# Kernel optimization log

Measured on AMD Instinct MI355X. Metric: run time of the kernel, lower is better.

Reference implementation:

```python
import jax, jax.numpy as jnp
import numpy as np

D = 128
EPS = 1e-5

def group_norm1(x, gamma, beta):
    # GroupNorm with num_groups=1 over channel dim of [N, C]
    mu = jnp.mean(x, axis=-1, keepdims=True)
    var = jnp.mean(jnp.square(x - mu), axis=-1, keepdims=True)
    xhat = (x - mu) * jax.lax.rsqrt(var + EPS)
    return xhat * gamma + beta

def setup_inputs() -> dict:
    key = jax.random.key(0)
    ks = jax.random.split(key, 12)
    N_ctx, N_tgt, E = 40000, 40000, 640000
    s = 0.09  # ~1/sqrt(128) weight scale
    inp = {
        'context_feat': jax.random.normal(ks[0], (N_ctx, D), jnp.float32),
        'target_feat': jax.random.normal(ks[1], (N_tgt, D), jnp.float32),
        'context_pose': jax.random.normal(ks[2], (N_ctx, 4), jnp.float32),
        'target_pose': jax.random.normal(ks[3], (N_tgt, 4), jnp.float32),
        'W_input': s * jax.random.normal(ks[4], (D, D), jnp.float32),
        'W_rp': 0.5 * jax.random.normal(ks[5], (4, D), jnp.float32),
        'b_rp': jnp.zeros((D,), jnp.float32),
        'W_c1': s * jax.random.normal(ks[6], (2 * D, D), jnp.float32),
        'g_c1': jnp.ones((D,), jnp.float32),
        'b_c1': jnp.zeros((D,), jnp.float32),
        'W_c2': s * jax.random.normal(ks[7], (D, D), jnp.float32),
        'g_n': jnp.ones((D,), jnp.float32),
        'b_n': jnp.zeros((D,), jnp.float32),
        'W_m1': s * jax.random.normal(ks[8], (D, D), jnp.float32),
        'g_m1': jnp.ones((D,), jnp.float32),
        'bm1': jnp.zeros((D,), jnp.float32),
        'W_m2': s * jax.random.normal(ks[9], (D, D), jnp.float32),
        'g_m2': jnp.ones((D,), jnp.float32),
        'bm2': jnp.zeros((D,), jnp.float32),
        'hi': jax.random.randint(ks[10], (E,), 0, N_ctx, jnp.int32),
        'wi': jax.random.randint(ks[11], (E,), 0, N_tgt, jnp.int32),
    }
    return inp

def reference(context_feat, target_feat, context_pose, target_pose,
              W_input, W_rp, b_rp, W_c1, g_c1, b_c1, W_c2,
              g_n, b_n, W_m1, g_m1, bm1, W_m2, g_m2, bm2, hi, wi):
    # relpose: Linear(4,128) + ReLU on relative pose of each (context, target) edge
    dist_feat = context_pose[hi] - target_pose[wi]                 # [E, 4]
    dist_feat = jax.nn.relu(dist_feat @ W_rp + b_rp)               # [E, 128]
    # ctx: Linear(256,128,GN,ReLU) -> Linear(128,128, no bias)
    ctx = jnp.concatenate([context_feat[hi], dist_feat], axis=-1)  # [E, 256]
    ctx = jax.nn.relu(group_norm1(ctx @ W_c1, g_c1, b_c1))
    ctx = ctx @ W_c2                                               # [E, 128]
    # input linear + index_add scatter into targets
    tf = target_feat @ W_input                                     # [N_tgt, 128]
    tf = tf + jax.ops.segment_sum(ctx, wi, num_segments=target_feat.shape[0])
    tf = jax.nn.relu(group_norm1(tf, g_n, b_n))
    # mlp: Linear(GN,ReLU) -> Linear(GN, no act)
    tf = jax.nn.relu(group_norm1(tf @ W_m1, g_m1, bm1))
    tf = group_norm1(tf @ W_m2, g_m2, bm2)
    # residual + relu
    return jax.nn.relu(tf + target_feat)
```

## Files before the change

### kernel.cpp

```cpp
#include <hip/hip_runtime.h>

#define D 128
#define EPSV 1e-5f

typedef __attribute__((ext_vector_type(8))) __bf16 bf16x8;
typedef __attribute__((ext_vector_type(4))) float f32x4;

__device__ __forceinline__ ushort f2bf(float x) {
  unsigned u = __float_as_uint(x);
  u += 0x7fffu + ((u >> 16) & 1u);
  return (ushort)(u >> 16);
}
__device__ __forceinline__ unsigned cvtpk(float lo, float hi) {
  unsigned r;
  asm("v_cvt_pk_bf16_f32 %0, %1, %2" : "=v"(r) : "v"(lo), "v"(hi));
  return r;
}
__device__ __forceinline__ int yidx(int row, int col) {
  return row * 128 + (col ^ ((row & 7) << 3));
}

__global__ void k_cvt(const float* __restrict__ Wc1, const float* __restrict__ Wc2,
                      ushort* __restrict__ WF1, ushort* __restrict__ WF2) {
  int o = blockIdx.x * 256 + threadIdx.x;
  if (o < 32768) {
    int j = o & 7, col = (o >> 3) & 127, gg = (o >> 10) & 3, kc = o >> 12;
    WF1[o] = f2bf(Wc1[(kc * 32 + gg * 8 + j) * 128 + col]);
  } else {
    int o2 = o - 32768;
    if (o2 < 16384) {
      int j = o2 & 7, col = (o2 >> 3) & 127, gg = (o2 >> 10) & 3, kc = o2 >> 12;
      WF2[o2] = f2bf(Wc2[(kc * 32 + gg * 8 + j) * 128 + col]);
    }
  }
}

__global__ void k_cvtf(const float* __restrict__ cf, ushort* __restrict__ cb,
                       int n8) {
  int i = blockIdx.x * 256 + threadIdx.x;
  if (i < n8) {
    float4 f0 = *(const float4*)(cf + (size_t)i * 8);
    float4 f1 = *(const float4*)(cf + (size_t)i * 8 + 4);
    uint4 p;
    p.x = cvtpk(f0.x, f0.y); p.y = cvtpk(f0.z, f0.w);
    p.z = cvtpk(f1.x, f1.y); p.w = cvtpk(f1.z, f1.w);
    *(uint4*)(cb + (size_t)i * 8) = p;
  }
}

__global__ void k_hist(const int* __restrict__ hi, int* __restrict__ hist, int E) {
  int i = blockIdx.x * 256 + threadIdx.x;
  if (i < E) atomicAdd(&hist[hi[i]], 1);
}

__global__ void k_scan1(const int* __restrict__ hist, int* __restrict__ bsum, int Nc) {
  __shared__ int sd[256];
  int t = threadIdx.x, i = blockIdx.x * 256 + t;
  sd[t] = (i < Nc) ? hist[i] : 0;
  __syncthreads();
  for (int off = 128; off > 0; off >>= 1) {
    if (t < off) sd[t] += sd[t + off];
    __syncthreads();
  }
  if (t == 0) bsum[blockIdx.x] = sd[0];
}

__global__ void k_scan2(const int* __restrict__ bsum, int* __restrict__ bpre, int nc) {
  __shared__ int sd[256];
  int t = threadIdx.x;
  int v = (t < nc) ? bsum[t] : 0;
  sd[t] = v;
  __syncthreads();
  for (int off = 1; off < 256; off <<= 1) {
    int x = (t >= off) ? sd[t - off] : 0;
    __syncthreads();
    sd[t] += x;
    __syncthreads();
  }
  if (t < nc) bpre[t] = sd[t] - v;
}

__global__ void k_scan3(const int* __restrict__ hist, const int* __restrict__ bpre,
                        int* __restrict__ cursor, int Nc) {
  __shared__ int sd[256];
  int t = threadIdx.x, i = blockIdx.x * 256 + t;
  int v = (i < Nc) ? hist[i] : 0;
  sd[t] = v;
  __syncthreads();
  for (int off = 1; off < 256; off <<= 1) {
    int x = (t >= off) ? sd[t - off] : 0;
    __syncthreads();
    sd[t] += x;
    __syncthreads();
  }
  if (i < Nc) cursor[i] = bpre[blockIdx.x] + sd[t] - v;
}

__global__ void k_order(const int* __restrict__ hi, const int* __restrict__ wi,
                        int* __restrict__ cursor,
                        int* __restrict__ hs, int* __restrict__ wt, int E) {
  int i = blockIdx.x * 256 + threadIdx.x;
  if (i < E) {
    int h = hi[i];
    int p = atomicAdd(&cursor[h], 1);
    hs[p] = h;
    wt[p] = wi[i];
  }
}

template <bool BF16CF>
__global__ __launch_bounds__(256, 4) void k_edge(
    const float* __restrict__ cfeat, const ushort* __restrict__ cfb,
    const float* __restrict__ cpose, const float* __restrict__ tpose,
    const float* __restrict__ Wrp, const float* __restrict__ brp,
    const float* __restrict__ gc1, const float* __restrict__ bc1,
    const ushort* __restrict__ WF1, const ushort* __restrict__ WF2,
    const int* __restrict__ he, const int* __restrict__ we,
    float* __restrict__ acc, int E) {
  __shared__ ushort Ybuf[128 * 128];
  __shared__ float gnbuf[2][128][2];
  __shared__ int wl[128];

  const int t = threadIdx.x;
  const int lane = t & 63;
  const int wv = t >> 6;
  const int wm = wv >> 1, wn = wv & 1;
  const int s = lane & 15, g = lane >> 4;
  const int e0 = blockIdx.x * 128;

  if (t < 128) wl[t] = we[min(e0 + t, E - 1)];

  int hl[4];
#pragma unroll
  for (int m = 0; m < 4; ++m)
    hl[m] = he[min(e0 + wm * 64 + m * 16 + s, E - 1)];

  {
    const int e = t >> 1;
    const int jh = (t & 1) * 64;
    const int ge = min(e0 + e, E - 1);
    const int h = he[ge], w = we[ge];
    float4 cp = *(const float4*)(cpose + (size_t)h * 4);
    float4 tp = *(const float4*)(tpose + (size_t)w * 4);
    const float d0 = cp.x - tp.x, d1 = cp.y - tp.y;
    const float d2 = cp.z - tp.z, d3 = cp.w - tp.w;
#pragma unroll
    for (int q = 0; q < 16; ++q) {
      const int j = jh + q * 4;
      float4 b  = *(const float4*)(brp + j);
      float4 w0 = *(const float4*)(Wrp + j);
      float4 w1 = *(const float4*)(Wrp + D + j);
      float4 w2 = *(const float4*)(Wrp + 2 * D + j);
      float4 w3 = *(const float4*)(Wrp + 3 * D + j);
      float r0 = fmaxf(b.x + d0 * w0.x + d1 * w1.x + d2 * w2.x + d3 * w3.x, 0.f);
      float r1 = fmaxf(b.y + d0 * w0.y + d1 * w1.y + d2 * w2.y + d3 * w3.y, 0.f);
      float r2 = fmaxf(b.z + d0 * w0.z + d1 * w1.z + d2 * w2.z + d3 * w3.z, 0.f);
      float r3 = fmaxf(b.w + d0 * w0.w + d1 * w1.w + d2 * w2.w + d3 * w3.w, 0.f);
      *(uint2*)&Ybuf[yidx(e, j)] = make_uint2(cvtpk(r0, r1), cvtpk(r2, r3));
    }
  }

  auto bfrag = [&](const ushort* WF, int kc, int n) {
    return *(const bf16x8*)&WF[(((kc * 4 + g) * 128) + wn * 64 + n * 16 + s) * 8];
  };

  f32x4 acc1[4][4];
#pragma unroll
  for (int m = 0; m < 4; ++m)
#pragma unroll
    for (int n = 0; n < 4; ++n) acc1[m][n] = (f32x4){0.f, 0.f, 0.f, 0.f};

  for (int kc = 0; kc < 4; ++kc) {
    bf16x8 a[4];
    if (BF16CF) {
#pragma unroll
      for (int m = 0; m < 4; ++m)
        a[m] = *(const bf16x8*)(cfb + (size_t)hl[m] * D + kc * 32 + g * 8);
    } else {
#pragma unroll
      for (int m = 0; m < 4; ++m) {
        const float* src = cfeat + (size_t)hl[m] * D + kc * 32 + g * 8;
        float4 f0 = *(const float4*)src;
        float4 f1 = *(const float4*)(src + 4);
        union { uint4 u; bf16x8 v; } cv;
        cv.u.x = cvtpk(f0.x, f0.y); cv.u.y = cvtpk(f0.z, f0.w);
        cv.u.z = cvtpk(f1.x, f1.y); cv.u.w = cvtpk(f1.z, f1.w);
        a[m] = cv.v;
      }
    }
#pragma unroll
    for (int n = 0; n < 4; ++n) {
      bf16x8 b = bfrag(WF1, kc, n);
#pragma unroll
      for (int m = 0; m < 4; ++m)
        acc1[m][n] =
            __builtin_amdgcn_mfma_f32_16x16x32_bf16(a[m], b, acc1[m][n], 0, 0, 0);
    }
  }

  __syncthreads();

  for (int kc = 4; kc < 8; ++kc) {
    bf16x8 a[4];
#pragma unroll
    for (int m = 0; m < 4; ++m)
      a[m] = *(const bf16x8*)
          &Ybuf[yidx(wm * 64 + m * 16 + s, (kc - 4) * 32 + g * 8)];
#pragma unroll
    for (int n = 0; n < 4; ++n) {
      bf16x8 b = bfrag(WF1, kc, n);
#pragma unroll
      for (int m = 0; m < 4; ++m)
        acc1[m][n] =
            __builtin_amdgcn_mfma_f32_16x16x32_bf16(a[m], b, acc1[m][n], 0, 0, 0);
    }
  }

#pragma unroll
  for (int m = 0; m < 4; ++m) {
#pragma unroll
    for (int reg = 0; reg < 4; ++reg) {
      float p1 = acc1[m][0][reg] + acc1[m][1][reg] + acc1[m][2][reg] +
                 acc1[m][3][reg];
      float p2 = acc1[m][0][reg] * acc1[m][0][reg] +
                 acc1[m][1][reg] * acc1[m][1][reg] +
                 acc1[m][2][reg] * acc1[m][2][reg] +
                 acc1[m][3][reg] * acc1[m][3][reg];
#pragma unroll
      for (int msk = 1; msk < 16; msk <<= 1) {
        p1 += __shfl_xor(p1, msk, 64);
        p2 += __shfl_xor(p2, msk, 64);
      }
      if (s == 0) {
        const int row = wm * 64 + m * 16 + g * 4 + reg;
        *(float2*)&gnbuf[wn][row][0] = make_float2(p1, p2);
      }
    }
  }
  __syncthreads();

  {
    float gcl[4], bcl[4];
#pragma unroll
    for (int n = 0; n < 4; ++n) {
      gcl[n] = gc1[wn * 64 + n * 16 + s];
      bcl[n] = bc1[wn * 64 + n * 16 + s];
    }
#pragma unroll
    for (int m = 0; m < 4; ++m) {
#pragma unroll
      for (int reg = 0; reg < 4; ++reg) {
        const int row = wm * 64 + m * 16 + g * 4 + reg;
        float2 q0 = *(const float2*)&gnbuf[0][row][0];
        float2 q1 = *(const float2*)&gnbuf[1][row][0];
        const float mean = (q0.x + q1.x) * (1.f / 128.f);
        const float var = (q0.y + q1.y) * (1.f / 128.f) - mean * mean;
        const float rstd = rsqrtf(var + EPSV);
#pragma unroll
        for (int n = 0; n < 4; ++n) {
          float y = fmaxf((acc1[m][n][reg] - mean) * rstd * gcl[n] + bcl[n], 0.f);
          Ybuf[yidx(row, wn * 64 + n * 16 + s)] = (ushort)cvtpk(y, y);
        }
      }
    }
  }
  __syncthreads();

  f32x4 acc2[4][4];
#pragma unroll
  for (int m = 0; m < 4; ++m)
#pragma unroll
    for (int n = 0; n < 4; ++n) acc2[m][n] = (f32x4){0.f, 0.f, 0.f, 0.f};

  for (int kc = 0; kc < 4; ++kc) {
    bf16x8 a[4];
#pragma unroll
    for (int m = 0; m < 4; ++m)
      a[m] = *(const bf16x8*)&Ybuf[yidx(wm * 64 + m * 16 + s, kc * 32 + g * 8)];
#pragma unroll
    for (int n = 0; n < 4; ++n) {
      bf16x8 b = bfrag(WF2, kc, n);
#pragma unroll
      for (int m = 0; m < 4; ++m)
        acc2[m][n] =
            __builtin_amdgcn_mfma_f32_16x16x32_bf16(a[m], b, acc2[m][n], 0, 0, 0);
    }
  }

#pragma unroll
  for (int m = 0; m < 4; ++m) {
#pragma unroll
    for (int reg = 0; reg < 4; ++reg) {
      const int rl = wm * 64 + m * 16 + g * 4 + reg;
      if (e0 + rl < E) {
        const int w = wl[rl];
        float* base = acc + (size_t)w * D + wn * 64 + s;
#pragma unroll
        for (int n = 0; n < 4; ++n)
          unsafeAtomicAdd(base + n * 16, acc2[m][n][reg]);
      }
    }
  }
}

__device__ __forceinline__ void reduce16(float& a, float& b) {
#pragma unroll
  for (int w = 1; w < 16; w <<= 1) {
    a += __shfl_xor(a, w, 64);
    b += __shfl_xor(b, w, 64);
  }
}

__global__ __launch_bounds__(256, 2) void k_input(
    const float* __restrict__ tfeat, const float* __restrict__ Wi,
    float* __restrict__ acc, int N) {
  __shared__ float Wbuf[64][132];
  __shared__ float xt[64][132];
  const int t = threadIdx.x;
  const int r = t >> 4, s = t & 15, j0 = s * 8;
  const int row0 = blockIdx.x * 64;

  for (int idx = t; idx < 64 * 32; idx += 256) {
    int rr = idx >> 5, c4 = idx & 31;
    int grow = row0 + rr;
    float4 v = make_float4(0.f, 0.f, 0.f, 0.f);
    if (grow < N) v = *(const float4*)(tfeat + (size_t)grow * D + c4 * 4);
    *(float4*)&xt[rr][c4 * 4] = v;
  }

  float a[4][8] = {};
  for (int kc = 0; kc < 2; ++kc) {
    __syncthreads();
    for (int idx = t; idx < 64 * 32; idx += 256) {
      int kk = idx >> 5, c4 = idx & 31;
      *(float4*)&Wbuf[kk][c4 * 4] =
          *(const float4*)(Wi + (size_t)(kc * 64 + kk) * D + c4 * 4);
    }
    __syncthreads();
#pragma unroll 4
    for (int kk = 0; kk < 64; ++kk) {
      float4 w0 = *(const float4*)&Wbuf[kk][j0];
      float4 w1 = *(const float4*)&Wbuf[kk][j0 + 4];
#pragma unroll
      for (int i = 0; i < 4; ++i) {
        float xv = xt[r + 16 * i][kc * 64 + kk];
        a[i][0] += xv * w0.x; a[i][1] += xv * w0.y;
        a[i][2] += xv * w0.z; a[i][3] += xv * w0.w;
        a[i][4] += xv * w1.x; a[i][5] += xv * w1.y;
        a[i][6] += xv * w1.z; a[i][7] += xv * w1.w;
      }
    }
  }
#pragma unroll
  for (int i = 0; i < 4; ++i) {
    int row = row0 + r + 16 * i;
    if (row < N) {
      *(float4*)(acc + (size_t)row * D + j0) =
          make_float4(a[i][0], a[i][1], a[i][2], a[i][3]);
      *(float4*)(acc + (size_t)row * D + j0 + 4) =
          make_float4(a[i][4], a[i][5], a[i][6], a[i][7]);
    }
  }
}

__global__ __launch_bounds__(256, 2) void k_node(
    const float* __restrict__ tfeat,
    const float* __restrict__ gn, const float* __restrict__ bn,
    const float* __restrict__ Wm1, const float* __restrict__ gm1,
    const float* __restrict__ bm1,
    const float* __restrict__ Wm2, const float* __restrict__ gm2,
    const float* __restrict__ bm2,
    float* __restrict__ acc, int N) {
  __shared__ float Wbuf[64][132];
  __shared__ float xt[64][132];
  const int t = threadIdx.x;
  const int r = t >> 4, s = t & 15, j0 = s * 8;
  const int row0 = blockIdx.x * 64;

  auto stageW = [&](const float* W, int kc) {
    for (int idx = t; idx < 64 * 32; idx += 256) {
      int kk = idx >> 5, c4 = idx & 31;
      *(float4*)&Wbuf[kk][c4 * 4] =
          *(const float4*)(W + (size_t)(kc * 64 + kk) * D + c4 * 4);
    }
  };
  auto gemm = [&](float (&a)[4][8], int kc) {
#pragma unroll 4
    for (int kk = 0; kk < 64; ++kk) {
      float4 w0 = *(const float4*)&Wbuf[kk][j0];
      float4 w1 = *(const float4*)&Wbuf[kk][j0 + 4];
#pragma unroll
      for (int i = 0; i < 4; ++i) {
        float xv = xt[r + 16 * i][kc * 64 + kk];
        a[i][0] += xv * w0.x; a[i][1] += xv * w0.y;
        a[i][2] += xv * w0.z; a[i][3] += xv * w0.w;
        a[i][4] += xv * w1.x; a[i][5] += xv * w1.y;
        a[i][6] += xv * w1.z; a[i][7] += xv * w1.w;
      }
    }
  };

  {
    float gv[8], bv[8];
#pragma unroll
    for (int m = 0; m < 8; ++m) { gv[m] = gn[j0 + m]; bv[m] = bn[j0 + m]; }
#pragma unroll
    for (int i = 0; i < 4; ++i) {
      int row = row0 + r + 16 * i;
      float v[8] = {};
      if (row < N) {
        float4 v0 = *(const float4*)(acc + (size_t)row * D + j0);
        float4 v1 = *(const float4*)(acc + (size_t)row * D + j0 + 4);
        v[0] = v0.x; v[1] = v0.y; v[2] = v0.z; v[3] = v0.w;
        v[4] = v1.x; v[5] = v1.y; v[6] = v1.z; v[7] = v1.w;
      }
      float s1 = 0.f, s2 = 0.f;
#pragma unroll
      for (int m = 0; m < 8; ++m) { s1 += v[m]; s2 += v[m] * v[m]; }
      reduce16(s1, s2);
      float mean = s1 * (1.f / 128.f);
      float var = s2 * (1.f / 128.f) - mean * mean;
      float rstd = rsqrtf(var + EPSV);
#pragma unroll
      for (int m = 0; m < 8; ++m)
        xt[r + 16 * i][j0 + m] = fmaxf((v[m] - mean) * rstd * gv[m] + bv[m], 0.f);
    }
  }

  float a[4][8] = {};
  for (int kc = 0; kc < 2; ++kc) {
    __syncthreads();
    stageW(Wm1, kc);
    __syncthreads();
    gemm(a, kc);
  }
  __syncthreads();
  {
    float gv[8], bv[8];
#pragma unroll
    for (int m = 0; m < 8; ++m) { gv[m] = gm1[j0 + m]; bv[m] = bm1[j0 + m]; }
#pragma unroll
    for (int i = 0; i < 4; ++i) {
      float s1 = 0.f, s2 = 0.f;
#pragma unroll
      for (int m = 0; m < 8; ++m) { s1 += a[i][m]; s2 += a[i][m] * a[i][m]; }
      reduce16(s1, s2);
      float mean = s1 * (1.f / 128.f);
      float var = s2 * (1.f / 128.f) - mean * mean;
      float rstd = rsqrtf(var + EPSV);
#pragma unroll
      for (int m = 0; m < 8; ++m)
        xt[r + 16 * i][j0 + m] =
            fmaxf((a[i][m] - mean) * rstd * gv[m] + bv[m], 0.f);
    }
  }

  float a2[4][8] = {};
  for (int kc = 0; kc < 2; ++kc) {
    __syncthreads();
    stageW(Wm2, kc);
    __syncthreads();
    gemm(a2, kc);
  }
  {
    float gv[8], bv[8];
#pragma unroll
    for (int m = 0; m < 8; ++m) { gv[m] = gm2[j0 + m]; bv[m] = bm2[j0 + m]; }
#pragma unroll
    for (int i = 0; i < 4; ++i) {
      int row = row0 + r + 16 * i;
      float s1 = 0.f, s2 = 0.f;
#pragma unroll
      for (int m = 0; m < 8; ++m) { s1 += a2[i][m]; s2 += a2[i][m] * a2[i][m]; }
      reduce16(s1, s2);
      float mean = s1 * (1.f / 128.f);
      float var = s2 * (1.f / 128.f) - mean * mean;
      float rstd = rsqrtf(var + EPSV);
      if (row < N) {
        float o[8];
#pragma unroll
        for (int m = 0; m < 8; ++m) {
          float x = (a2[i][m] - mean) * rstd * gv[m] + bv[m];
          o[m] = fmaxf(x + tfeat[(size_t)row * D + j0 + m], 0.f);
        }
        *(float4*)(acc + (size_t)row * D + j0) =
            make_float4(o[0], o[1], o[2], o[3]);
        *(float4*)(acc + (size_t)row * D + j0 + 4) =
            make_float4(o[4], o[5], o[6], o[7]);
      }
    }
  }
}

extern "C" void kernel_launch(void* const* d_in, const int* in_sizes, int n_in,
                              void* d_out, int out_size, void* d_ws,
                              size_t ws_size, hipStream_t stream) {
  const float* cfeat = (const float*)d_in[0];
  const float* tfeat = (const float*)d_in[1];
  const float* cpose = (const float*)d_in[2];
  const float* tpose = (const float*)d_in[3];
  const float* Wi    = (const float*)d_in[4];
  const float* Wrp   = (const float*)d_in[5];
  const float* brp   = (const float*)d_in[6];
  const float* Wc1   = (const float*)d_in[7];
  const float* gc1   = (const float*)d_in[8];
  const float* bc1   = (const float*)d_in[9];
  const float* Wc2   = (const float*)d_in[10];
  const float* gn    = (const float*)d_in[11];
  const float* bn    = (const float*)d_in[12];
  const float* Wm1   = (const float*)d_in[13];
  const float* gm1   = (const float*)d_in[14];
  const float* bm1   = (const float*)d_in[15];
  const float* Wm2   = (const float*)d_in[16];
  const float* gm2   = (const float*)d_in[17];
  const float* bm2   = (const float*)d_in[18];
  const int* hi      = (const int*)d_in[19];
  const int* wi      = (const int*)d_in[20];

  const int N  = in_sizes[1] / D;
  const int NC = in_sizes[0] / D;
  const int E  = in_sizes[19];
  const int CFE = in_sizes[0];
  float* out = (float*)d_out;

  uint8_t* ws = (uint8_t*)d_ws;
  ushort* WF1 = (ushort*)ws;
  ushort* WF2 = (ushort*)(ws + 65536);
  int* hist   = (int*)(ws + 98304);
  int* cursor = hist + NC;
  int* bsum   = cursor + NC;
  int* bpre   = bsum + 256;
  int* hs     = bpre + 256;
  int* wt     = hs + E;
  const size_t sort_end =
      98304 + ((size_t)2 * NC + 512 + (size_t)2 * E) * 4;
  ushort* cfb = (ushort*)(ws + ((sort_end + 255) & ~(size_t)255));
  const size_t cfb_end = ((sort_end + 255) & ~(size_t)255) + (size_t)CFE * 2;

  const int nchunksC = (NC + 255) / 256;
  const bool sorted = (ws_size >= sort_end) && (nchunksC <= 256);
  const bool bf16cf = ws_size >= cfb_end;

  const int nbN = (N + 63) / 64;
  const int nbE = (E + 127) / 128;
  const int nbEthr = (E + 255) / 256;

  if (sorted) {
    hipMemsetAsync(hist, 0, (size_t)NC * 4, stream);
    k_hist<<<nbEthr, 256, 0, stream>>>(hi, hist, E);
    k_scan1<<<nchunksC, 256, 0, stream>>>(hist, bsum, NC);
    k_scan2<<<1, 256, 0, stream>>>(bsum, bpre, nchunksC);
    k_scan3<<<nchunksC, 256, 0, stream>>>(hist, bpre, cursor, NC);
    k_order<<<nbEthr, 256, 0, stream>>>(hi, wi, cursor, hs, wt, E);
  }

  k_cvt<<<192, 256, 0, stream>>>(Wc1, Wc2, WF1, WF2);
  if (bf16cf)
    k_cvtf<<<(CFE / 8 + 255) / 256, 256, 0, stream>>>(cfeat, cfb, CFE / 8);
  k_input<<<nbN, 256, 0, stream>>>(tfeat, Wi, out, N);

  const int* he = sorted ? hs : hi;
  const int* we = sorted ? wt : wi;
  if (bf16cf)
    k_edge<true><<<nbE, 256, 0, stream>>>(cfeat, cfb, cpose, tpose, Wrp, brp,
                                          gc1, bc1, WF1, WF2, he, we, out, E);
  else
    k_edge<false><<<nbE, 256, 0, stream>>>(cfeat, cfb, cpose, tpose, Wrp, brp,
                                           gc1, bc1, WF1, WF2, he, we, out, E);
  k_node<<<nbN, 256, 0, stream>>>(tfeat, gn, bn, Wm1, gm1, bm1, Wm2, gm2, bm2,
                                  out, N);
}
```

Baseline: 523.1 us.

## Sort edges by target into CSR and accumulate per-target tiles in shared memory

Edges are now counting-sorted by target index instead of context index, producing a row pointer array. Each block owns 32 targets, processes their edge range in 128-edge chunks, and accumulates the second-linear outputs into a shared-memory tile with LDS atomics. It then adds the tile to the output with plain loads and stores. This removes the global float atomics on the scatter, at the cost of losing source-row locality for the context-feature gathers, uneven per-block work, and lower occupancy from the extra shared memory. The edge kernel now only runs when the workspace is large enough, leaving no fallback.

```diff
diff --git a/kernel.cpp b/kernel.cpp
--- a/kernel.cpp
+++ b/kernel.cpp
@@ -48,9 +48,9 @@
   }
 }
 
-__global__ void k_hist(const int* __restrict__ hi, int* __restrict__ hist, int E) {
+__global__ void k_hist(const int* __restrict__ wi, int* __restrict__ hist, int E) {
   int i = blockIdx.x * 256 + threadIdx.x;
-  if (i < E) atomicAdd(&hist[hi[i]], 1);
+  if (i < E) atomicAdd(&hist[wi[i]], 1);
 }
 
 __global__ void k_scan1(const int* __restrict__ hist, int* __restrict__ bsum, int Nc) {
@@ -81,7 +81,7 @@
 }
 
 __global__ void k_scan3(const int* __restrict__ hist, const int* __restrict__ bpre,
-                        int* __restrict__ cursor, int Nc) {
+                        int* __restrict__ cursor, int* __restrict__ rowptr, int Nc) {
   __shared__ int sd[256];
   int t = threadIdx.x, i = blockIdx.x * 256 + t;
   int v = (i < Nc) ? hist[i] : 0;
@@ -93,7 +93,11 @@
     sd[t] += x;
     __syncthreads();
   }
-  if (i < Nc) cursor[i] = bpre[blockIdx.x] + sd[t] - v;
+  if (i < Nc) {
+    int e = bpre[blockIdx.x] + sd[t] - v;
+    cursor[i] = e;
+    rowptr[i] = e;
+  }
 }
 
 __global__ void k_order(const int* __restrict__ hi, const int* __restrict__ wi,
@@ -101,23 +105,25 @@
                         int* __restrict__ hs, int* __restrict__ wt, int E) {
   int i = blockIdx.x * 256 + threadIdx.x;
   if (i < E) {
-    int h = hi[i];
-    int p = atomicAdd(&cursor[h], 1);
-    hs[p] = h;
-    wt[p] = wi[i];
+    int w = wi[i];
+    int p = atomicAdd(&cursor[w], 1);
+    hs[p] = hi[i];
+    wt[p] = w;
   }
 }
 
 template <bool BF16CF>
-__global__ __launch_bounds__(256, 4) void k_edge(
+__global__ __launch_bounds__(256, 3) void k_edge(
     const float* __restrict__ cfeat, const ushort* __restrict__ cfb,
     const float* __restrict__ cpose, const float* __restrict__ tpose,
     const float* __restrict__ Wrp, const float* __restrict__ brp,
     const float* __restrict__ gc1, const float* __restrict__ bc1,
     const ushort* __restrict__ WF1, const ushort* __restrict__ WF2,
-    const int* __restrict__ he, const int* __restrict__ we,
-    float* __restrict__ acc, int E) {
+    const int* __restrict__ hs, const int* __restrict__ wt,
+    const int* __restrict__ rowptr,
+    float* __restrict__ out, int N, int E) {
   __shared__ ushort Ybuf[128 * 128];
+  __shared__ float Abuf[32 * 128];
   __shared__ float gnbuf[2][128][2];
   __shared__ int wl[128];
 
@@ -126,179 +132,199 @@
   const int wv = t >> 6;
   const int wm = wv >> 1, wn = wv & 1;
   const int s = lane & 15, g = lane >> 4;
-  const int e0 = blockIdx.x * 128;
-
-  if (t < 128) wl[t] = we[min(e0 + t, E - 1)];
-
-  int hl[4];
-#pragma unroll
-  for (int m = 0; m < 4; ++m)
-    hl[m] = he[min(e0 + wm * 64 + m * 16 + s, E - 1)];
-
-  {
-    const int e = t >> 1;
-    const int jh = (t & 1) * 64;
-    const int ge = min(e0 + e, E - 1);
-    const int h = he[ge], w = we[ge];
-    float4 cp = *(const float4*)(cpose + (size_t)h * 4);
-    float4 tp = *(const float4*)(tpose + (size_t)w * 4);
-    const float d0 = cp.x - tp.x, d1 = cp.y - tp.y;
-    const float d2 = cp.z - tp.z, d3 = cp.w - tp.w;
-#pragma unroll
-    for (int q = 0; q < 16; ++q) {
-      const int j = jh + q * 4;
-      float4 b  = *(const float4*)(brp + j);
-      float4 w0 = *(const float4*)(Wrp + j);
-      float4 w1 = *(const float4*)(Wrp + D + j);
-      float4 w2 = *(const float4*)(Wrp + 2 * D + j);
-      float4 w3 = *(const float4*)(Wrp + 3 * D + j);
-      float r0 = fmaxf(b.x + d0 * w0.x + d1 * w1.x + d2 * w2.x + d3 * w3.x, 0.f);
-      float r1 = fmaxf(b.y + d0 * w0.y + d1 * w1.y + d2 * w2.y + d3 * w3.y, 0.f);
-      float r2 = fmaxf(b.z + d0 * w0.z + d1 * w1.z + d2 * w2.z + d3 * w3.z, 0.f);
-      float r3 = fmaxf(b.w + d0 * w0.w + d1 * w1.w + d2 * w2.w + d3 * w3.w, 0.f);
-      *(uint2*)&Ybuf[yidx(e, j)] = make_uint2(cvtpk(r0, r1), cvtpk(r2, r3));
-    }
-  }
+  const int t0 = blockIdx.x * 32;
+
+  const int rS = rowptr[t0];
+  const int rE = (t0 + 32 < N) ? rowptr[t0 + 32] : E;
+
+  for (int i = t; i < 1024; i += 256) ((float4*)Abuf)[i] = make_float4(0, 0, 0, 0);
 
   auto bfrag = [&](const ushort* WF, int kc, int n) {
     return *(const bf16x8*)&WF[(((kc * 4 + g) * 128) + wn * 64 + n * 16 + s) * 8];
   };
 
-  f32x4 acc1[4][4];
-#pragma unroll
-  for (int m = 0; m < 4; ++m)
-#pragma unroll
-    for (int n = 0; n < 4; ++n) acc1[m][n] = (f32x4){0.f, 0.f, 0.f, 0.f};
-
-  for (int kc = 0; kc < 4; ++kc) {
-    bf16x8 a[4];
-    if (BF16CF) {
+  for (int eb = rS; eb < rE; eb += 128) {
+    if (t < 128) wl[t] = wt[min(eb + t, rE - 1)];
+
+    int hl[4];
+#pragma unroll
+    for (int m = 0; m < 4; ++m)
+      hl[m] = hs[min(eb + wm * 64 + m * 16 + s, rE - 1)];
+
+    {
+      const int e = t >> 1;
+      const int jh = (t & 1) * 64;
+      const int ge = min(eb + e, rE - 1);
+      const int h = hs[ge], w = wt[ge];
+      float4 cp = *(const float4*)(cpose + (size_t)h * 4);
+      float4 tp = *(const float4*)(tpose + (size_t)w * 4);
+      const float d0 = cp.x - tp.x, d1 = cp.y - tp.y;
+      const float d2 = cp.z - tp.z, d3 = cp.w - tp.w;
+#pragma unroll
+      for (int q = 0; q < 16; ++q) {
+        const int j = jh + q * 4;
+        float4 b  = *(const float4*)(brp + j);
+        float4 w0 = *(const float4*)(Wrp + j);
+        float4 w1 = *(const float4*)(Wrp + D + j);
+        float4 w2 = *(const float4*)(Wrp + 2 * D + j);
+        float4 w3 = *(const float4*)(Wrp + 3 * D + j);
+        float r0 = fmaxf(b.x + d0 * w0.x + d1 * w1.x + d2 * w2.x + d3 * w3.x, 0.f);
+        float r1 = fmaxf(b.y + d0 * w0.y + d1 * w1.y + d2 * w2.y + d3 * w3.y, 0.f);
+        float r2 = fmaxf(b.z + d0 * w0.z + d1 * w1.z + d2 * w2.z + d3 * w3.z, 0.f);
+        float r3 = fmaxf(b.w + d0 * w0.w + d1 * w1.w + d2 * w2.w + d3 * w3.w, 0.f);
+        *(uint2*)&Ybuf[yidx(e, j)] = make_uint2(cvtpk(r0, r1), cvtpk(r2, r3));
+      }
+    }
+
+    f32x4 acc1[4][4];
+#pragma unroll
+    for (int m = 0; m < 4; ++m)
+#pragma unroll
+      for (int n = 0; n < 4; ++n) acc1[m][n] = (f32x4){0.f, 0.f, 0.f, 0.f};
+
+    for (int kc = 0; kc < 4; ++kc) {
+      bf16x8 a[4];
+      if (BF16CF) {
+#pragma unroll
+        for (int m = 0; m < 4; ++m)
+          a[m] = *(const bf16x8*)(cfb + (size_t)hl[m] * D + kc * 32 + g * 8);
+      } else {
+#pragma unroll
+        for (int m = 0; m < 4; ++m) {
+          const float* src = cfeat + (size_t)hl[m] * D + kc * 32 + g * 8;
+          float4 f0 = *(const float4*)src;
+          float4 f1 = *(const float4*)(src + 4);
+          union { uint4 u; bf16x8 v; } cv;
+          cv.u.x = cvtpk(f0.x, f0.y); cv.u.y = cvtpk(f0.z, f0.w);
+          cv.u.z = cvtpk(f1.x, f1.y); cv.u.w = cvtpk(f1.z, f1.w);
+          a[m] = cv.v;
+        }
+      }
+#pragma unroll
+      for (int n = 0; n < 4; ++n) {
+        bf16x8 b = bfrag(WF1, kc, n);
+#pragma unroll
+        for (int m = 0; m < 4; ++m)
+          acc1[m][n] =
+              __builtin_amdgcn_mfma_f32_16x16x32_bf16(a[m], b, acc1[m][n], 0, 0, 0);
+      }
+    }
+
+    __syncthreads();
+
+    for (int kc = 4; kc < 8; ++kc) {
+      bf16x8 a[4];
 #pragma unroll
       for (int m = 0; m < 4; ++m)
-        a[m] = *(const bf16x8*)(cfb + (size_t)hl[m] * D + kc * 32 + g * 8);
-    } else {
+        a[m] = *(const bf16x8*)
+            &Ybuf[yidx(wm * 64 + m * 16 + s, (kc - 4) * 32 + g * 8)];
+#pragma unroll
+      for (int n = 0; n < 4; ++n) {
+        bf16x8 b = bfrag(WF1, kc, n);
+#pragma unroll
+        for (int m = 0; m < 4; ++m)
+          acc1[m][n] =
+              __builtin_amdgcn_mfma_f32_16x16x32_bf16(a[m], b, acc1[m][n], 0, 0, 0);
+      }
+    }
+
+#pragma unroll
+    for (int m = 0; m < 4; ++m) {
+#pragma unroll
+      for (int reg = 0; reg < 4; ++reg) {
+        float p1 = acc1[m][0][reg] + acc1[m][1][reg] + acc1[m][2][reg] +
+                   acc1[m][3][reg];
+        float p2 = acc1[m][0][reg] * acc1[m][0][reg] +
+                   acc1[m][1][reg] * acc1[m][1][reg] +
+                   acc1[m][2][reg] * acc1[m][2][reg] +
+                   acc1[m][3][reg] * acc1[m][3][reg];
+#pragma unroll
+        for (int msk = 1; msk < 16; msk <<= 1) {
+          p1 += __shfl_xor(p1, msk, 64);
+          p2 += __shfl_xor(p2, msk, 64);
+        }
+        if (s == 0) {
+          const int row = wm * 64 + m * 16 + g * 4 + reg;
+          *(float2*)&gnbuf[wn][row][0] = make_float2(p1, p2);
+        }
+      }
+    }
+    __syncthreads();
+
+    {
+      float gcl[4], bcl[4];
+#pragma unroll
+      for (int n = 0; n < 4; ++n) {
+        gcl[n] = gc1[wn * 64 + n * 16 + s];
+        bcl[n] = bc1[wn * 64 + n * 16 + s];
+      }
 #pragma unroll
       for (int m = 0; m < 4; ++m) {
-        const float* src = cfeat + (size_t)hl[m] * D + kc * 32 + g * 8;
-        float4 f0 = *(const float4*)src;
-        float4 f1 = *(const float4*)(src + 4);
-        union { uint4 u; bf16x8 v; } cv;
-        cv.u.x = cvtpk(f0.x, f0.y); cv.u.y = cvtpk(f0.z, f0.w);
-        cv.u.z = cvtpk(f1.x, f1.y); cv.u.w = cvtpk(f1.z, f1.w);
-        a[m] = cv.v;
-      }
-    }
-#pragma unroll
-    for (int n = 0; n < 4; ++n) {
-      bf16x8 b = bfrag(WF1, kc, n);
+#pragma unroll
+        for (int reg = 0; reg < 4; ++reg) {
+          const int row = wm * 64 + m * 16 + g * 4 + reg;
+          float2 q0 = *(const float2*)&gnbuf[0][row][0];
+          float2 q1 = *(const float2*)&gnbuf[1][row][0];
+          const float mean = (q0.x + q1.x) * (1.f / 128.f);
+          const float var = (q0.y + q1.y) * (1.f / 128.f) - mean * mean;
+          const float rstd = rsqrtf(var + EPSV);
+#pragma unroll
+          for (int n = 0; n < 4; ++n) {
+            float y = fmaxf((acc1[m][n][reg] - mean) * rstd * gcl[n] + bcl[n], 0.f);
+            Ybuf[yidx(row, wn * 64 + n * 16 + s)] = (ushort)cvtpk(y, y);
+          }
+        }
+      }
+    }
+    __syncthreads();
+
+    f32x4 acc2[4][4];
+#pragma unroll
+    for (int m = 0; m < 4; ++m)
+#pragma unroll
+      for (int n = 0; n < 4; ++n) acc2[m][n] = (f32x4){0.f, 0.f, 0.f, 0.f};
+
+    for (int kc = 0; kc < 4; ++kc) {
+      bf16x8 a[4];
 #pragma unroll
       for (int m = 0; m < 4; ++m)
-        acc1[m][n] =
-            __builtin_amdgcn_mfma_f32_16x16x32_bf16(a[m], b, acc1[m][n], 0, 0, 0);
-    }
-  }
-
-  __syncthreads();
-
-  for (int kc = 4; kc < 8; ++kc) {
-    bf16x8 a[4];
-#pragma unroll
-    for (int m = 0; m < 4; ++m)
-      a[m] = *(const bf16x8*)
-          &Ybuf[yidx(wm * 64 + m * 16 + s, (kc - 4) * 32 + g * 8)];
-#pragma unroll
-    for (int n = 0; n < 4; ++n) {
-      bf16x8 b = bfrag(WF1, kc, n);
-#pragma unroll
-      for (int m = 0; m < 4; ++m)
-        acc1[m][n] =
-            __builtin_amdgcn_mfma_f32_16x16x32_bf16(a[m], b, acc1[m][n], 0, 0, 0);
-    }
-  }
-
-#pragma unroll
-  for (int m = 0; m < 4; ++m) {
-#pragma unroll
-    for (int reg = 0; reg < 4; ++reg) {
-      float p1 = acc1[m][0][reg] + acc1[m][1][reg] + acc1[m][2][reg] +
-                 acc1[m][3][reg];
-      float p2 = acc1[m][0][reg] * acc1[m][0][reg] +
-                 acc1[m][1][reg] * acc1[m][1][reg] +
-                 acc1[m][2][reg] * acc1[m][2][reg] +
-                 acc1[m][3][reg] * acc1[m][3][reg];
-#pragma unroll
-      for (int msk = 1; msk < 16; msk <<= 1) {
-        p1 += __shfl_xor(p1, msk, 64);
-        p2 += __shfl_xor(p2, msk, 64);
-      }
-      if (s == 0) {
-        const int row = wm * 64 + m * 16 + g * 4 + reg;
-        *(float2*)&gnbuf[wn][row][0] = make_float2(p1, p2);
-      }
-    }
-  }
-  __syncthreads();
-
-  {
-    float gcl[4], bcl[4];
-#pragma unroll
-    for (int n = 0; n < 4; ++n) {
-      gcl[n] = gc1[wn * 64 + n * 16 + s];
-      bcl[n] = bc1[wn * 64 + n * 16 + s];
-    }
+        a[m] = *(const bf16x8*)&Ybuf[yidx(wm * 64 + m * 16 + s, kc * 32 + g * 8)];
+#pragma unroll
+      for (int n = 0; n < 4; ++n) {
+        bf16x8 b = bfrag(WF2, kc, n);
+#pragma unroll
+        for (int m = 0; m < 4; ++m)
+          acc2[m][n] =
+              __builtin_amdgcn_mfma_f32_16x16x32_bf16(a[m], b, acc2[m][n], 0, 0, 0);
+      }
+    }
+
 #pragma unroll
     for (int m = 0; m < 4; ++m) {
 #pragma unroll
       for (int reg = 0; reg < 4; ++reg) {
         const int row = wm * 64 + m * 16 + g * 4 + reg;
-        float2 q0 = *(const float2*)&gnbuf[0][row][0];
-        float2 q1 = *(const float2*)&gnbuf[1][row][0];
-        const float mean = (q0.x + q1.x) * (1.f / 128.f);
-        const float var = (q0.y + q1.y) * (1.f / 128.f) - mean * mean;
-        const float rstd = rsqrtf(var + EPSV);
-#pragma unroll
-        for (int n = 0; n < 4; ++n) {
-          float y = fmaxf((acc1[m][n][reg] - mean) * rstd * gcl[n] + bcl[n], 0.f);
-          Ybuf[yidx(row, wn * 64 + n * 16 + s)] = (ushort)cvtpk(y, y);
+        if (eb + row < rE) {
+          const int tl = wl[row] - t0;
+          float* base = &Abuf[tl * 128 + wn * 64 + s];
+#pragma unroll
+          for (int n = 0; n < 4; ++n)
+            atomicAdd(base + n * 16, acc2[m][n][reg]);
         }
       }
     }
-  }
-  __syncthreads();
-
-  f32x4 acc2[4][4];
-#pragma unroll
-  for (int m = 0; m < 4; ++m)
-#pragma unroll
-    for (int n = 0; n < 4; ++n) acc2[m][n] = (f32x4){0.f, 0.f, 0.f, 0.f};
-
-  for (int kc = 0; kc < 4; ++kc) {
-    bf16x8 a[4];
-#pragma unroll
-    for (int m = 0; m < 4; ++m)
-      a[m] = *(const bf16x8*)&Ybuf[yidx(wm * 64 + m * 16 + s, kc * 32 + g * 8)];
-#pragma unroll
-    for (int n = 0; n < 4; ++n) {
-      bf16x8 b = bfrag(WF2, kc, n);
-#pragma unroll
-      for (int m = 0; m < 4; ++m)
-        acc2[m][n] =
-            __builtin_amdgcn_mfma_f32_16x16x32_bf16(a[m], b, acc2[m][n], 0, 0, 0);
-    }
-  }
-
-#pragma unroll
-  for (int m = 0; m < 4; ++m) {
-#pragma unroll
-    for (int reg = 0; reg < 4; ++reg) {
-      const int rl = wm * 64 + m * 16 + g * 4 + reg;
-      if (e0 + rl < E) {
-        const int w = wl[rl];
-        float* base = acc + (size_t)w * D + wn * 64 + s;
-#pragma unroll
-        for (int n = 0; n < 4; ++n)
-          unsafeAtomicAdd(base + n * 16, acc2[m][n][reg]);
-      }
+    __syncthreads();
+  }
+
+  for (int i = t; i < 1024; i += 256) {
+    const int tl = i >> 5, c4 = i & 31;
+    const int row = t0 + tl;
+    if (row < N) {
+      float* dst = out + (size_t)row * D + c4 * 4;
+      float4 o = *(float4*)dst;
+      float4 a = ((float4*)Abuf)[i];
+      o.x += a.x; o.y += a.y; o.z += a.z; o.w += a.w;
+      *(float4*)dst = o;
     }
   }
 }
@@ -518,7 +544,6 @@
   const int* wi      = (const int*)d_in[20];
 
   const int N  = in_sizes[1] / D;
-  const int NC = in_sizes[0] / D;
   const int E  = in_sizes[19];
   const int CFE = in_sizes[0];
   float* out = (float*)d_out;
@@ -527,46 +552,48 @@
   ushort* WF1 = (ushort*)ws;
   ushort* WF2 = (ushort*)(ws + 65536);
   int* hist   = (int*)(ws + 98304);
-  int* cursor = hist + NC;
-  int* bsum   = cursor + NC;
+  int* cursor = hist + N;
+  int* rowptr = cursor + N;
+  int* bsum   = rowptr + N;
   int* bpre   = bsum + 256;
   int* hs     = bpre + 256;
   int* wt     = hs + E;
   const size_t sort_end =
-      98304 + ((size_t)2 * NC + 512 + (size_t)2 * E) * 4;
+      98304 + ((size_t)3 * N + 512 + (size_t)2 * E) * 4;
   ushort* cfb = (ushort*)(ws + ((sort_end + 255) & ~(size_t)255));
   const size_t cfb_end = ((sort_end + 255) & ~(size_t)255) + (size_t)CFE * 2;
 
-  const int nchunksC = (NC + 255) / 256;
-  const bool sorted = (ws_size >= sort_end) && (nchunksC <= 256);
+  const int nchunks = (N + 255) / 256;
+  const bool csr = (ws_size >= sort_end) && (nchunks <= 256);
   const bool bf16cf = ws_size >= cfb_end;
 
   const int nbN = (N + 63) / 64;
-  const int nbE = (E + 127) / 128;
   const int nbEthr = (E + 255) / 256;
-
-  if (sorted) {
-    hipMemsetAsync(hist, 0, (size_t)NC * 4, stream);
-    k_hist<<<nbEthr, 256, 0, stream>>>(hi, hist, E);
-    k_scan1<<<nchunksC, 256, 0, stream>>>(hist, bsum, NC);
-    k_scan2<<<1, 256, 0, stream>>>(bsum, bpre, nchunksC);
-    k_scan3<<<nchunksC, 256, 0, stream>>>(hist, bpre, cursor, NC);
-    k_order<<<nbEthr, 256, 0, stream>>>(hi, wi, cursor, hs, wt, E);
-  }
 
   k_cvt<<<192, 256, 0, stream>>>(Wc1, Wc2, WF1, WF2);
   if (bf16cf)
     k_cvtf<<<(CFE / 8 + 255) / 256, 256, 0, stream>>>(cfeat, cfb, CFE / 8);
   k_input<<<nbN, 256, 0, stream>>>(tfeat, Wi, out, N);
 
-  const int* he = sorted ? hs : hi;
-  const int* we = sorted ? wt : wi;
-  if (bf16cf)
-    k_edge<true><<<nbE, 256, 0, stream>>>(cfeat, cfb, cpose, tpose, Wrp, brp,
-                                          gc1, bc1, WF1, WF2, he, we, out, E);
-  else
-    k_edge<false><<<nbE, 256, 0, stream>>>(cfeat, cfb, cpose, tpose, Wrp, brp,
-                                           gc1, bc1, WF1, WF2, he, we, out, E);
+  if (csr) {
+    hipMemsetAsync(hist, 0, (size_t)N * 4, stream);
+    k_hist<<<nbEthr, 256, 0, stream>>>(wi, hist, E);
+    k_scan1<<<nchunks, 256, 0, stream>>>(hist, bsum, N);
+    k_scan2<<<1, 256, 0, stream>>>(bsum, bpre, nchunks);
+    k_scan3<<<nchunks, 256, 0, stream>>>(hist, bpre, cursor, rowptr, N);
+    k_order<<<nbEthr, 256, 0, stream>>>(hi, wi, cursor, hs, wt, E);
+
+    const int nbT = (N + 31) / 32;
+    if (bf16cf)
+      k_edge<true><<<nbT, 256, 0, stream>>>(cfeat, cfb, cpose, tpose, Wrp, brp,
+                                            gc1, bc1, WF1, WF2, hs, wt, rowptr,
+                                            out, N, E);
+    else
+      k_edge<false><<<nbT, 256, 0, stream>>>(cfeat, cfb, cpose, tpose, Wrp, brp,
+                                             gc1, bc1, WF1, WF2, hs, wt, rowptr,
+                                             out, N, E);
+  }
+
   k_node<<<nbN, 256, 0, stream>>>(tfeat, gn, bn, Wm1, gm1, bm1, Wm2, gm2, bm2,
                                   out, N);
 }
```

New measurement: 1.108 ms. 112% more time.
